# Optimization experiments

Measured on AMD Instinct MI355X. Metric: run time of the kernel, lower is better.

The kernel has to match this reference:

```python
import jax, jax.numpy as jnp
import numpy as np

# Static video grid (F, H, W); S = F*H*W tokens.
F_FRAMES, H_GRID, W_GRID = 9, 16, 28
DIM, N_HEADS = 1536, 12
HEAD_DIM = DIM // N_HEADS          # 128
ROT = HEAD_DIM // 2                # 64 complex pairs
EPS = 1e-6


def setup_inputs() -> dict:
    key = jax.random.key(0)
    ks = jax.random.split(key, 12)
    S = F_FRAMES * H_GRID * W_GRID
    scale = 0.02
    inp = {
        "x": jax.random.normal(ks[0], (1, S, DIM), jnp.float32),
        "seq_lens": jnp.array([S], jnp.int32),
        "grid_sizes": jnp.array([[F_FRAMES, H_GRID, W_GRID]], jnp.int32),
        "freqs": jax.random.normal(ks[1], (1024, ROT), jnp.float32),  # rope angles
        "Wq": jax.random.normal(ks[2], (DIM, DIM), jnp.float32) * scale,
        "bq": jnp.zeros((DIM,), jnp.float32),
        "Wk": jax.random.normal(ks[3], (DIM, DIM), jnp.float32) * scale,
        "bk": jnp.zeros((DIM,), jnp.float32),
        "Wv": jax.random.normal(ks[4], (DIM, DIM), jnp.float32) * scale,
        "bv": jnp.zeros((DIM,), jnp.float32),
        "Wo": jax.random.normal(ks[5], (DIM, DIM), jnp.float32) * scale,
        "bo": jnp.zeros((DIM,), jnp.float32),
        "gq": jnp.ones((DIM,), jnp.float32),
        "gk": jnp.ones((DIM,), jnp.float32),
    }
    return inp


def _rms_norm(h, g):
    # WanRMSNorm: h * rsqrt(mean(h^2) + eps) * weight
    var = jnp.mean(jnp.square(h), axis=-1, keepdims=True)
    return h * jax.lax.rsqrt(var + EPS) * g


def _rope_angles(freqs):
    # Split channel dim into temporal / height / width parts.
    c = ROT
    t_dim = c - 2 * (c // 3)  # 22
    s1 = c // 3               # 21
    temporal, height, width = freqs[:, :t_dim], freqs[:, t_dim:t_dim + s1], freqs[:, t_dim + s1:]
    t_ang = jnp.repeat(temporal[:F_FRAMES], H_GRID * W_GRID, axis=0)         # [S, 22]
    h_ang = jnp.tile(jnp.repeat(height[:H_GRID], W_GRID, axis=0), (F_FRAMES, 1))  # [S, 21]
    w_ang = jnp.tile(jnp.tile(width[:W_GRID], (H_GRID, 1)), (F_FRAMES, 1))        # [S, 21]
    return jnp.concatenate([t_ang, h_ang, w_ang], axis=-1)  # [S, c]


def _rope_apply(x, ang):
    # x: [B, S, n, d] viewed as complex pairs [B, S, n, d/2, 2]
    b, s, n, d = x.shape
    xp = x.reshape(b, s, n, d // 2, 2)
    xr, xi = xp[..., 0], xp[..., 1]
    cos = jnp.cos(ang)[None, :, None, :]
    sin = jnp.sin(ang)[None, :, None, :]
    out_r = xr * cos - xi * sin
    out_i = xr * sin + xi * cos
    return jnp.stack([out_r, out_i], axis=-1).reshape(b, s, n, d)


def reference(x, seq_lens, grid_sizes, freqs, Wq, bq, Wk, bk, Wv, bv, Wo, bo, gq, gk):
    b, s, _ = x.shape
    n, d = N_HEADS, HEAD_DIM
    q = _rms_norm(x @ Wq + bq, gq).reshape(b, s, n, d)
    k = _rms_norm(x @ Wk + bk, gk).reshape(b, s, n, d)
    v = (x @ Wv + bv).reshape(b, s, n, d)

    ang = _rope_angles(freqs)  # [S, d/2]
    rq = _rope_apply(q, ang)
    rk = _rope_apply(k, ang)

    # Causal frame-block mask: query in frame i attends to kv in frames <= i.
    frame_idx = jnp.arange(s) // (H_GRID * W_GRID)
    mask = frame_idx[None, :] <= frame_idx[:, None]  # [S_q, S_k]

    scale = 1.0 / jnp.sqrt(jnp.asarray(d, x.dtype))
    scores = jnp.einsum("bqnd,bknd->bnqk", rq, rk) * scale
    scores = jnp.where(mask[None, None], scores, jnp.asarray(-1e30, scores.dtype))
    probs = jax.nn.softmax(scores, axis=-1)
    attn = jnp.einsum("bnqk,bknd->bqnd", probs, v).reshape(b, s, n * d)
    return attn @ Wo + bo
```

## Files before the change

### kernel.cpp

```cpp
#include <hip/hip_runtime.h>
#include <stdint.h>

typedef unsigned short u16;
typedef unsigned int u32;
typedef __attribute__((ext_vector_type(8))) short bf16x8;
typedef __attribute__((ext_vector_type(4))) float f32x4;

#define S_LEN 4032
#define S_PAD 4096
#define DIMC  1536
#define HD    128
#define FRAME 448

static const size_t OFF_FLAG  = 0;
static const size_t OFF_CANON = 256;
static const size_t OFF_XB    = 524288;
static const size_t OFF_WT    = OFF_XB  + 12582912;
static const size_t OFF_WOT   = OFF_WT  + 14155776;
static const size_t OFF_YQ    = OFF_WOT + 4718592;
static const size_t OFF_YK    = OFF_YQ  + 12582912;
static const size_t OFF_VT    = OFF_YK  + 12582912;
static const size_t OFF_QH    = OFF_VT  + 12582912;
static const size_t OFF_KH    = OFF_QH  + 12386304;
static const size_t OFF_AT    = OFF_KH  + 12386304;
static const size_t WS_NEED   = OFF_AT  + 12582912;

#define C_BQ 0
#define C_BO 4608
#define C_GQ 6144
#define C_GK 7680
#define C_FR 9216
#define C_TOT 74752

__device__ __forceinline__ u16 f2bf(float f) {
  union { float f; u32 u; } v; v.f = f;
  u32 u = v.u;
  u32 r = (u + 0x7fffu + ((u >> 16) & 1u)) >> 16;
  return (u16)r;
}
__device__ __forceinline__ float bf2f(u16 h) {
  union { float f; u32 u; } v; v.u = ((u32)h) << 16;
  return v.f;
}
__device__ __forceinline__ u32 cvtpk(float a, float b) {
  u32 r;
  asm("v_cvt_pk_bf16_f32 %0, %1, %2" : "=v"(r) : "v"(a), "v"(b));
  return r;
}

__device__ __forceinline__ void gld_lds16(const void* g, void* l) {
  __builtin_amdgcn_global_load_lds(
      (const __attribute__((address_space(1))) void*)(uintptr_t)g,
      (__attribute__((address_space(3))) void*)(u32)(uintptr_t)l,
      16, 0, 0);
}

__device__ __forceinline__ f32x4 mfma16(bf16x8 a, bf16x8 b, f32x4 c) {
  return __builtin_amdgcn_mfma_f32_16x16x32_bf16(a, b, c, 0, 0, 0);
}

#define WAITV8() asm volatile("s_waitcnt vmcnt(8)" ::: "memory")
#define WAITV0() asm volatile("s_waitcnt vmcnt(0)" ::: "memory")
#define BAR()    __builtin_amdgcn_s_barrier()

__global__ void prep_all(const void* __restrict__ x,
                         const void* Wq, const void* Wk, const void* Wv, const void* Wo,
                         const void* bq, const void* bk, const void* bv, const void* bo,
                         const void* gq, const void* gk, const void* fr,
                         float* __restrict__ canon, u16* __restrict__ xb,
                         u16* __restrict__ wqkvt, u16* __restrict__ wot,
                         int* __restrict__ flag) {
  __shared__ int cnt;
  __shared__ float tile[32][33];
  const int tid = threadIdx.x;
  if (tid == 0) cnt = 0;
  __syncthreads();
  int e = (((const u16*)x)[2 * tid] >> 7) & 0xff;
  if (e > 150) atomicAdd(&cnt, 1);
  __syncthreads();
  const int fl = (cnt >= 8) ? 1 : 0;
  const int bid = blockIdx.x;
  if (bid == 0 && tid == 0) *flag = fl;

  if (bid < 9216) {
    const int z = bid / 2304;
    const int rem = bid % 2304;
    const int by = rem / 48, bx = rem % 48;
    const void* W = (z == 0) ? Wq : (z == 1) ? Wk : (z == 2) ? Wv : Wo;
    u16* dst = (z < 3) ? (wqkvt + (size_t)z * DIMC * DIMC) : wot;
    const int tx = tid & 31, ty = tid >> 5;
    const int c = bx * 32 + tx;
    #pragma unroll
    for (int i = 0; i < 4; i++) {
      int r = by * 32 + ty + i * 8;
      float v = fl ? ((const float*)W)[(size_t)r * DIMC + c]
                   : bf2f(((const u16*)W)[(size_t)r * DIMC + c]);
      tile[ty + i * 8][tx] = v;
    }
    __syncthreads();
    const int k = by * 32 + tx;
    #pragma unroll
    for (int i = 0; i < 4; i++) {
      int n = bx * 32 + ty + i * 8;
      dst[(size_t)n * DIMC + k] = f2bf(tile[tx][ty + i * 8]);
    }
  } else if (bid < 12288) {
    int i = (bid - 9216) * 256 + tid;
    if (i < (S_PAD * DIMC) / 8) {
      size_t base = (size_t)i * 8;
      int row = (int)(base / DIMC);
      uint4 v;
      if (row < S_LEN) {
        if (fl) {
          const float4* xf = (const float4*)((const float*)x + base);
          float4 a = xf[0], b2 = xf[1];
          union { u16 h[8]; uint4 v; } u;
          u.h[0] = f2bf(a.x);  u.h[1] = f2bf(a.y);
          u.h[2] = f2bf(a.z);  u.h[3] = f2bf(a.w);
          u.h[4] = f2bf(b2.x); u.h[5] = f2bf(b2.y);
          u.h[6] = f2bf(b2.z); u.h[7] = f2bf(b2.w);
          v = u.v;
        } else {
          v = *(const uint4*)((const u16*)x + base);
        }
      } else {
        v = make_uint4(0u, 0u, 0u, 0u);
      }
      ((uint4*)xb)[i] = v;
    }
  } else {
    for (int i = (bid - 12288) * 256 + tid; i < C_TOT; i += 292 * 256) {
      const void* src; int j;
      if      (i < 1536) { src = bq; j = i; }
      else if (i < 3072) { src = bk; j = i - 1536; }
      else if (i < 4608) { src = bv; j = i - 3072; }
      else if (i < 6144) { src = bo; j = i - 4608; }
      else if (i < 7680) { src = gq; j = i - 6144; }
      else if (i < 9216) { src = gk; j = i - 7680; }
      else               { src = fr; j = i - 9216; }
      canon[i] = fl ? ((const float*)src)[j] : bf2f(((const u16*)src)[j]);
    }
  }
}

template <int MODE>
__launch_bounds__(256, 4)
__global__ void gemm_bt(const u16* __restrict__ A, const u16* __restrict__ Bt,
                        const float* __restrict__ canon,
                        u16* __restrict__ Yq, u16* __restrict__ Yk, u16* __restrict__ Vt,
                        void* __restrict__ Out, const int* __restrict__ flagp) {
  constexpr int nbx = (MODE == 0) ? 36 : 12;
  constexpr int nwg = nbx * 32;
  const int bid = blockIdx.x + blockIdx.y * nbx;
  const int swz = (bid & 7) * (nwg >> 3) + (bid >> 3);
  const int bm0 = (swz / nbx) * 128, bn0 = (swz % nbx) * 128;
  const int tid = threadIdx.x, wave = tid >> 6, lane = tid & 63;
  const int wm = wave >> 1, wn = wave & 1;
  const int l15 = lane & 15, l4 = lane >> 4;
  __shared__ u16 sA[128 * 64];
  __shared__ u16 sB[128 * 64];
  f32x4 acc[4][4];
  #pragma unroll
  for (int i = 0; i < 4; i++)
    #pragma unroll
    for (int j = 0; j < 4; j++) acc[i][j] = (f32x4){0.f, 0.f, 0.f, 0.f};

  const int swc = ((lane & 7) ^ (lane >> 3)) * 8;
  const u16* Ab = A  + (size_t)(bm0 + (lane >> 3)) * DIMC + swc;
  const u16* Bb = Bt + (size_t)(bn0 + (lane >> 3)) * DIMC + swc;

  for (int kt = 0; kt < DIMC; kt += 64) {
    __syncthreads();
    #pragma unroll
    for (int c = 0; c < 4; c++) {
      int g = wave * 4 + c;
      gld_lds16(Ab + (size_t)g * 8 * DIMC + kt, (char*)sA + g * 1024);
      gld_lds16(Bb + (size_t)g * 8 * DIMC + kt, (char*)sB + g * 1024);
    }
    __syncthreads();
    #pragma unroll
    for (int ks = 0; ks < 2; ks++) {
      bf16x8 av[4], bvv[4];
      #pragma unroll
      for (int mt = 0; mt < 4; mt++)
        av[mt]  = *(const bf16x8*)(sA + (wm * 64 + mt * 16 + l15) * 64 +
                                   (((ks * 4 + l4) ^ (l15 & 7)) * 8));
      #pragma unroll
      for (int nt = 0; nt < 4; nt++)
        bvv[nt] = *(const bf16x8*)(sB + (wn * 64 + nt * 16 + l15) * 64 +
                                   (((ks * 4 + l4) ^ (l15 & 7)) * 8));
      #pragma unroll
      for (int mt = 0; mt < 4; mt++)
        #pragma unroll
        for (int nt = 0; nt < 4; nt++)
          acc[mt][nt] = mfma16(av[mt], bvv[nt], acc[mt][nt]);
    }
  }

  const int gm0 = bm0 + wm * 64;
  const int gn0 = bn0 + wn * 64;
  if (MODE == 0) {
    #pragma unroll
    for (int nt = 0; nt < 4; nt++) {
      int gn = gn0 + nt * 16 + l15;
      float b = canon[C_BQ + gn];
      #pragma unroll
      for (int mt = 0; mt < 4; mt++) {
        int gm = gm0 + mt * 16 + l4 * 4;
        if (gn < 1536) {
          #pragma unroll
          for (int r = 0; r < 4; r++)
            Yq[(size_t)(gm + r) * DIMC + gn] = f2bf(acc[mt][nt][r] + b);
        } else if (gn < 3072) {
          int g2 = gn - 1536;
          #pragma unroll
          for (int r = 0; r < 4; r++)
            Yk[(size_t)(gm + r) * DIMC + g2] = f2bf(acc[mt][nt][r] + b);
        } else {
          int g2 = gn - 3072;
          uint2 pk;
          pk.x = cvtpk(acc[mt][nt][0] + b, acc[mt][nt][1] + b);
          pk.y = cvtpk(acc[mt][nt][2] + b, acc[mt][nt][3] + b);
          *(uint2*)(Vt + (size_t)g2 * S_PAD + gm) = pk;
        }
      }
    }
  } else {
    const int fl = *flagp;
    #pragma unroll
    for (int nt = 0; nt < 4; nt++) {
      int gn = gn0 + nt * 16 + l15;
      float b = canon[C_BO + gn];
      #pragma unroll
      for (int mt = 0; mt < 4; mt++) {
        int gm = gm0 + mt * 16 + l4 * 4;
        #pragma unroll
        for (int r = 0; r < 4; r++) {
          int gr = gm + r;
          if (gr < S_LEN) {
            float v = acc[mt][nt][r] + b;
            if (fl) ((float*)Out)[(size_t)gr * DIMC + gn] = v;
            else    ((u16*)Out)[(size_t)gr * DIMC + gn] = f2bf(v);
          }
        }
      }
    }
  }
}

__global__ void norm_rope(const u16* __restrict__ Yq, const u16* __restrict__ Yk,
                          const float* __restrict__ canon, u16* __restrict__ Qh,
                          u16* __restrict__ Kh) {
  const int tid = threadIdx.x, wave = tid >> 6, lane = tid & 63;
  const int s = blockIdx.x * 4 + wave;
  const int isq = (blockIdx.y == 0);
  const u16* Y = isq ? Yq : Yk;
  const float* g = canon + (isq ? C_GQ : C_GK);
  u16* Oh = isq ? Qh : Kh;
  const float sc = isq ? (0.08838834764831845f * 1.4426950408889634f) : 1.0f;

  const u32* yrow = (const u32*)Y + (size_t)s * 768;
  float xr[12], xi[12];
  float ss = 0.f;
  #pragma unroll
  for (int i = 0; i < 12; i++) {
    u32 d = yrow[lane + 64 * i];
    float a = bf2f((u16)(d & 0xffff));
    float b = bf2f((u16)(d >> 16));
    xr[i] = a; xi[i] = b;
    ss += a * a + b * b;
  }
  #pragma unroll
  for (int dd = 1; dd < 64; dd <<= 1) ss += __shfl_xor(ss, dd, 64);
  float rms = rsqrtf(ss * (1.f / 1536.f) + 1e-6f);

  int f_ = s / FRAME, hh = (s % FRAME) / 28, ww = s % 28;
  const float* fr = canon + C_FR;
  float a = (lane < 22) ? fr[f_ * 64 + lane]
          : (lane < 43) ? fr[hh * 64 + lane]
                        : fr[ww * 64 + lane];
  float si, co;
  __sincosf(a, &si, &co);

  const float2* g2 = (const float2*)g;
  #pragma unroll
  for (int i = 0; i < 12; i++) {
    int p = lane + 64 * i;
    float2 gg = g2[p];
    float r  = xr[i] * rms * gg.x;
    float im = xi[i] * rms * gg.y;
    u32 pk = cvtpk((r * co - im * si) * sc, (r * si + im * co) * sc);
    ((u32*)Oh)[((size_t)i * S_LEN + s) * 64 + lane] = pk;
  }
}

__launch_bounds__(256, 2)
__global__ void attn_v12(const u16* __restrict__ Qh, const u16* __restrict__ Kh,
                         const u16* __restrict__ Vt, u16* __restrict__ Ab) {
  const int serial = ((int)blockIdx.x & 7) * 96 + ((int)blockIdx.x >> 3);
  const int h = serial >> 6;
  const int qs = serial & 63;
  if (qs == 63) return;
  const int qb = (qs & 1) ? (qs >> 1) : (62 - (qs >> 1));
  const int q0 = qb * 64;
  const int nkv = (q0 / FRAME + 1) * 7;
  const int tid = threadIdx.x, wave = tid >> 6, lane = tid & 63;
  const int l15 = lane & 15, l4 = lane >> 4;
  const int qh = wave >> 1;
  const int kh = wave & 1;
  __shared__ u16 sK[2][8192];
  __shared__ u16 sV[2][8192];

  int koff[4], voff[4];
  #pragma unroll
  for (int i = 0; i < 4; i++) {
    int c = i * 256 + tid;
    int r = c >> 4, cc = (c & 15) ^ (r & 15);
    koff[i] = r * HD + cc * 8;
    int rv = c >> 3, cv = (c & 7) ^ (rv & 7);
    voff[i] = rv * S_PAD + cv * 8;
  }

  bf16x8 qf[4][2];
  {
    const u16* qp = Qh + ((size_t)h * S_LEN + q0 + qh * 32 + l15) * HD + l4 * 8;
    #pragma unroll
    for (int f = 0; f < 2; f++)
      #pragma unroll
      for (int ks = 0; ks < 4; ks++)
        qf[ks][f] = *(const bf16x8*)(qp + f * 16 * HD + ks * 32);
  }
  f32x4 o[8][2];
  #pragma unroll
  for (int i = 0; i < 8; i++)
    #pragma unroll
    for (int f = 0; f < 2; f++) o[i][f] = (f32x4){0.f, 0.f, 0.f, 0.f};
  float l_i[2] = {0.f, 0.f};

  const u16* kb0 = Kh + (size_t)h * S_LEN * HD;
  const u16* vb0 = Vt + (size_t)h * HD * S_PAD;

  #pragma unroll
  for (int i = 0; i < 4; i++) {
    gld_lds16(kb0 + koff[i], (char*)sK[0] + i * 4096 + wave * 1024);
    gld_lds16(vb0 + voff[i], (char*)sV[0] + i * 4096 + wave * 1024);
  }

  for (int t = 0; t < nkv; ++t) {
    const int cur = t & 1;
    if (t + 1 < nkv) {
      const u16* kb = kb0 + (size_t)(t + 1) * 64 * HD;
      const u16* vb = vb0 + (t + 1) * 64;
      #pragma unroll
      for (int i = 0; i < 4; i++) {
        gld_lds16(kb + koff[i], (char*)sK[cur ^ 1] + i * 4096 + wave * 1024);
        gld_lds16(vb + voff[i], (char*)sV[cur ^ 1] + i * 4096 + wave * 1024);
      }
      WAITV8();
    } else {
      WAITV0();
    }
    BAR();

    f32x4 sT[2][2];
    #pragma unroll
    for (int nt = 0; nt < 2; nt++)
      #pragma unroll
      for (int f = 0; f < 2; f++) sT[nt][f] = (f32x4){0.f, 0.f, 0.f, 0.f};
    __builtin_amdgcn_s_setprio(1);
    #pragma unroll
    for (int ks = 0; ks < 4; ks++) {
      bf16x8 kf[2];
      #pragma unroll
      for (int nt = 0; nt < 2; nt++)
        kf[nt] = *(const bf16x8*)(sK[cur] + (kh * 32 + nt * 16 + l15) * HD +
                                  (((ks * 4 + l4) ^ l15) * 8));
      #pragma unroll
      for (int nt = 0; nt < 2; nt++)
        #pragma unroll
        for (int f = 0; f < 2; f++)
          sT[nt][f] = mfma16(kf[nt], qf[ks][f], sT[nt][f]);
    }
    __builtin_amdgcn_s_setprio(0);

    bf16x8 pb[2];
    #pragma unroll
    for (int f = 0; f < 2; f++) {
      float rs = 0.f;
      #pragma unroll
      for (int nt = 0; nt < 2; nt++)
        #pragma unroll
        for (int r = 0; r < 4; r++) {
          float p = __builtin_amdgcn_exp2f(sT[nt][f][r]);
          sT[nt][f][r] = p; rs += p;
        }
      l_i[f] += rs;
      u32 ax = cvtpk(sT[0][f][0], sT[0][f][1]);
      u32 bx = cvtpk(sT[1][f][0], sT[1][f][1]);
      u32 ay = cvtpk(sT[0][f][2], sT[0][f][3]);
      u32 by = cvtpk(sT[1][f][2], sT[1][f][3]);
      asm volatile("v_permlane32_swap_b32 %0, %1" : "+v"(ax), "+v"(bx));
      asm volatile("v_permlane16_swap_b32 %0, %1" : "+v"(ax), "+v"(bx));
      asm volatile("v_permlane32_swap_b32 %0, %1" : "+v"(ay), "+v"(by));
      asm volatile("v_permlane16_swap_b32 %0, %1" : "+v"(ay), "+v"(by));
      union { u32 w[4]; bf16x8 v; } u;
      u.w[0] = ax; u.w[1] = ay; u.w[2] = bx; u.w[3] = by;
      pb[f] = u.v;
    }

    __builtin_amdgcn_s_setprio(1);
    #pragma unroll
    for (int vt = 0; vt < 8; vt++) {
      bf16x8 vf = *(const bf16x8*)(sV[cur] + (vt * 16 + l15) * 64 +
                                   (((kh * 4 + l4) ^ (l15 & 7)) * 8));
      #pragma unroll
      for (int f = 0; f < 2; f++)
        o[vt][f] = mfma16(vf, pb[f], o[vt][f]);
    }
    __builtin_amdgcn_s_setprio(0);

    BAR();
  }

  #pragma unroll
  for (int f = 0; f < 2; f++) {
    l_i[f] += __shfl_xor(l_i[f], 16, 64);
    l_i[f] += __shfl_xor(l_i[f], 32, 64);
  }
  float* mb = (float*)sK;
  float* lb = (float*)sV;
  __syncthreads();
  if (kh == 1) {
    #pragma unroll
    for (int f = 0; f < 2; f++) {
      #pragma unroll
      for (int vt = 0; vt < 8; vt++)
        *(f32x4*)(mb + qh * 4096 + (f * 8 + vt) * 256 + lane * 4) = o[vt][f];
      lb[qh * 128 + f * 64 + lane] = l_i[f];
    }
  }
  __syncthreads();
  if (kh == 0) {
    #pragma unroll
    for (int f = 0; f < 2; f++) {
      float l = l_i[f] + lb[qh * 128 + f * 64 + lane];
      float inv = 1.f / l;
      const size_t orow = (size_t)(q0 + qh * 32 + f * 16 + l15) * DIMC + (size_t)h * HD;
      #pragma unroll
      for (int vt = 0; vt < 8; vt++) {
        f32x4 op = *(const f32x4*)(mb + qh * 4096 + (f * 8 + vt) * 256 + lane * 4);
        uint2 pk;
        pk.x = cvtpk((o[vt][f][0] + op[0]) * inv, (o[vt][f][1] + op[1]) * inv);
        pk.y = cvtpk((o[vt][f][2] + op[2]) * inv, (o[vt][f][3] + op[3]) * inv);
        *(uint2*)(Ab + orow + vt * 16 + l4 * 4) = pk;
      }
    }
  }
}

extern "C" void kernel_launch(void* const* d_in, const int* in_sizes, int n_in,
                              void* d_out, int out_size, void* d_ws, size_t ws_size,
                              hipStream_t stream) {
  if (ws_size < WS_NEED) return;
  char* ws = (char*)d_ws;
  int*   flag  = (int*)(ws + OFF_FLAG);
  float* canon = (float*)(ws + OFF_CANON);
  u16* xb    = (u16*)(ws + OFF_XB);
  u16* wqkvt = (u16*)(ws + OFF_WT);
  u16* wot   = (u16*)(ws + OFF_WOT);
  u16* yq    = (u16*)(ws + OFF_YQ);
  u16* yk    = (u16*)(ws + OFF_YK);
  u16* vt    = (u16*)(ws + OFF_VT);
  u16* qh    = (u16*)(ws + OFF_QH);
  u16* kh    = (u16*)(ws + OFF_KH);
  u16* ab    = (u16*)(ws + OFF_AT);

  const void* x  = d_in[0];
  const void* fr = d_in[3];
  const void* Wq = d_in[4];  const void* bq = d_in[5];
  const void* Wk = d_in[6];  const void* bk = d_in[7];
  const void* Wv = d_in[8];  const void* bv = d_in[9];
  const void* Wo = d_in[10]; const void* bo = d_in[11];
  const void* gq = d_in[12]; const void* gk = d_in[13];

  prep_all<<<12580, 256, 0, stream>>>(x, Wq, Wk, Wv, Wo, bq, bk, bv, bo, gq, gk, fr,
                                      canon, xb, wqkvt, wot, flag);
  gemm_bt<0><<<dim3(36, 32), 256, 0, stream>>>(xb, wqkvt, canon, yq, yk, vt, nullptr, flag);
  norm_rope<<<dim3(1008, 2), 256, 0, stream>>>(yq, yk, canon, qh, kh);
  attn_v12<<<768, 256, 0, stream>>>(qh, kh, vt, ab);
  gemm_bt<1><<<dim3(12, 32), 256, 0, stream>>>(ab, wot, canon, nullptr, nullptr, nullptr, d_out, flag);
}
```

Measured before the change: 374.1 us.

## Load K fragments directly to registers, drop K LDS staging, raise occupancy

The attention kernel stops staging K tiles through LDS. Each wave now loads its K MFMA fragments straight from global memory into registers, and only V stays double-buffered in LDS. This halves shared memory, so launch bounds rise to 3 blocks per CU, and the explicit vmcnt waits are replaced by __syncthreads. The block mapping is also simplified to heaviest-first ordering (q block 62 downward) with exactly 756 blocks instead of a strided mapping with a dead slot. The cost is duplicated K global reads across the two query-half waves and exposed global load latency in the inner loop.

```diff
diff --git a/kernel.cpp b/kernel.cpp
--- a/kernel.cpp
+++ b/kernel.cpp
@@ -58,10 +58,6 @@
 __device__ __forceinline__ f32x4 mfma16(bf16x8 a, bf16x8 b, f32x4 c) {
   return __builtin_amdgcn_mfma_f32_16x16x32_bf16(a, b, c, 0, 0, 0);
 }
-
-#define WAITV8() asm volatile("s_waitcnt vmcnt(8)" ::: "memory")
-#define WAITV0() asm volatile("s_waitcnt vmcnt(0)" ::: "memory")
-#define BAR()    __builtin_amdgcn_s_barrier()
 
 __global__ void prep_all(const void* __restrict__ x,
                          const void* Wq, const void* Wk, const void* Wv, const void* Wo,
@@ -294,29 +290,24 @@
   }
 }
 
-__launch_bounds__(256, 2)
-__global__ void attn_v12(const u16* __restrict__ Qh, const u16* __restrict__ Kh,
+__launch_bounds__(256, 3)
+__global__ void attn_v14(const u16* __restrict__ Qh, const u16* __restrict__ Kh,
                          const u16* __restrict__ Vt, u16* __restrict__ Ab) {
-  const int serial = ((int)blockIdx.x & 7) * 96 + ((int)blockIdx.x >> 3);
-  const int h = serial >> 6;
-  const int qs = serial & 63;
-  if (qs == 63) return;
-  const int qb = (qs & 1) ? (qs >> 1) : (62 - (qs >> 1));
-  const int q0 = qb * 64;
-  const int nkv = (q0 / FRAME + 1) * 7;
   const int tid = threadIdx.x, wave = tid >> 6, lane = tid & 63;
   const int l15 = lane & 15, l4 = lane >> 4;
   const int qh = wave >> 1;
   const int kh = wave & 1;
-  __shared__ u16 sK[2][8192];
+  const int h = blockIdx.x % 12;
+  const int qb = 62 - (blockIdx.x / 12);
+  const int q0 = qb * 64;
+  const int nkv = (q0 / FRAME + 1) * 7;
   __shared__ u16 sV[2][8192];
-
-  int koff[4], voff[4];
+  __shared__ float lb[256];
+
+  int voff[4];
   #pragma unroll
   for (int i = 0; i < 4; i++) {
     int c = i * 256 + tid;
-    int r = c >> 4, cc = (c & 15) ^ (r & 15);
-    koff[i] = r * HD + cc * 8;
     int rv = c >> 3, cv = (c & 7) ^ (rv & 7);
     voff[i] = rv * S_PAD + cv * 8;
   }
@@ -337,30 +328,30 @@
     for (int f = 0; f < 2; f++) o[i][f] = (f32x4){0.f, 0.f, 0.f, 0.f};
   float l_i[2] = {0.f, 0.f};
 
-  const u16* kb0 = Kh + (size_t)h * S_LEN * HD;
+  const u16* kfb = Kh + ((size_t)h * S_LEN + kh * 32 + l15) * HD + l4 * 8;
   const u16* vb0 = Vt + (size_t)h * HD * S_PAD;
 
   #pragma unroll
-  for (int i = 0; i < 4; i++) {
-    gld_lds16(kb0 + koff[i], (char*)sK[0] + i * 4096 + wave * 1024);
+  for (int i = 0; i < 4; i++)
     gld_lds16(vb0 + voff[i], (char*)sV[0] + i * 4096 + wave * 1024);
-  }
+  __syncthreads();
 
   for (int t = 0; t < nkv; ++t) {
     const int cur = t & 1;
+    const u16* kp = kfb + (size_t)t * 64 * HD;
+    bf16x8 kfr[2][4];
+    #pragma unroll
+    for (int nt = 0; nt < 2; nt++)
+      #pragma unroll
+      for (int ks = 0; ks < 4; ks++)
+        kfr[nt][ks] = *(const bf16x8*)(kp + nt * 16 * HD + ks * 32);
+
     if (t + 1 < nkv) {
-      const u16* kb = kb0 + (size_t)(t + 1) * 64 * HD;
       const u16* vb = vb0 + (t + 1) * 64;
       #pragma unroll
-      for (int i = 0; i < 4; i++) {
-        gld_lds16(kb + koff[i], (char*)sK[cur ^ 1] + i * 4096 + wave * 1024);
+      for (int i = 0; i < 4; i++)
         gld_lds16(vb + voff[i], (char*)sV[cur ^ 1] + i * 4096 + wave * 1024);
-      }
-      WAITV8();
-    } else {
-      WAITV0();
-    }
-    BAR();
+    }
 
     f32x4 sT[2][2];
     #pragma unroll
@@ -369,18 +360,12 @@
       for (int f = 0; f < 2; f++) sT[nt][f] = (f32x4){0.f, 0.f, 0.f, 0.f};
     __builtin_amdgcn_s_setprio(1);
     #pragma unroll
-    for (int ks = 0; ks < 4; ks++) {
-      bf16x8 kf[2];
-      #pragma unroll
-      for (int nt = 0; nt < 2; nt++)
-        kf[nt] = *(const bf16x8*)(sK[cur] + (kh * 32 + nt * 16 + l15) * HD +
-                                  (((ks * 4 + l4) ^ l15) * 8));
+    for (int ks = 0; ks < 4; ks++)
       #pragma unroll
       for (int nt = 0; nt < 2; nt++)
         #pragma unroll
         for (int f = 0; f < 2; f++)
-          sT[nt][f] = mfma16(kf[nt], qf[ks][f], sT[nt][f]);
-    }
+          sT[nt][f] = mfma16(kfr[nt][ks], qf[ks][f], sT[nt][f]);
     __builtin_amdgcn_s_setprio(0);
 
     bf16x8 pb[2];
@@ -419,7 +404,7 @@
     }
     __builtin_amdgcn_s_setprio(0);
 
-    BAR();
+    __syncthreads();
   }
 
   #pragma unroll
@@ -427,9 +412,7 @@
     l_i[f] += __shfl_xor(l_i[f], 16, 64);
     l_i[f] += __shfl_xor(l_i[f], 32, 64);
   }
-  float* mb = (float*)sK;
-  float* lb = (float*)sV;
-  __syncthreads();
+  float* mb = (float*)sV;
   if (kh == 1) {
     #pragma unroll
     for (int f = 0; f < 2; f++) {
@@ -487,6 +470,6 @@
                                       canon, xb, wqkvt, wot, flag);
   gemm_bt<0><<<dim3(36, 32), 256, 0, stream>>>(xb, wqkvt, canon, yq, yk, vt, nullptr, flag);
   norm_rope<<<dim3(1008, 2), 256, 0, stream>>>(yq, yk, canon, qh, kh);
-  attn_v12<<<768, 256, 0, stream>>>(qh, kh, vt, ab);
+  attn_v14<<<756, 256, 0, stream>>>(qh, kh, vt, ab);
   gemm_bt<1><<<dim3(12, 32), 256, 0, stream>>>(ab, wot, canon, nullptr, nullptr, nullptr, d_out, flag);
 }
```

Measured after the change: 399.1 us. 6.7% more time.
